# Performance work log

Measured on AMD Instinct MI355X. Metric: run time of the kernel, lower is better.

The kernel has to match this reference:

```python
import jax, jax.numpy as jnp
import numpy as np

B = 131072
MOTION_DIM = 512


def setup_inputs() -> dict:
    key = jax.random.key(0)
    k1, k2 = jax.random.split(key)
    inp = jax.random.normal(k1, (B, MOTION_DIM), dtype=jnp.float32)
    weight = jax.random.normal(k2, (512, MOTION_DIM), dtype=jnp.float32)
    return {"input": inp, "weight": weight}


def reference(input, weight):
    # weight: (512, motion_dim); reduced QR -> Q: (512, motion_dim)
    Q, R = jnp.linalg.qr(weight + 1e-8)
    # Original: sum_i diag(input)[b] @ Q.T over dim=1 == input @ Q.T
    # out[b, n] = sum_m input[b, m] * Q[n, m]
    out = jnp.einsum("bm,nm->bn", input, Q)  # (B, 512)
    return out
```

## Files before the change

### kernel.cpp

```cpp
#include <hip/hip_runtime.h>
#include <hip/hip_bf16.h>

#define NN 512
#define NB 32
#define NPANELS 16
#define BDIM 256
#define PF_BDIM 512
#define LB_BDIM 512


__device__ inline unsigned short f2bf(float x) {
    unsigned int u = __float_as_uint(x);
    return (unsigned short)((u + 0x7FFFu + ((u >> 16) & 1u)) >> 16);
}

__global__ __launch_bounds__(BDIM)
void prep_kernel(const float* __restrict__ W, float* __restrict__ A, float* __restrict__ Q)
{
    int idx = blockIdx.x * BDIM + threadIdx.x;
    if (idx < NN * NN) {
        A[idx] = W[idx] + 1e-8f;
        int r = idx >> 9, c = idx & (NN - 1);
        Q[idx] = (r == c) ? 1.0f : 0.0f;
    }
}

__global__ __launch_bounds__(PF_BDIM)
void panel_fact(float* __restrict__ A, float* __restrict__ Vbuf,
                float* __restrict__ tau, float* __restrict__ Tbuf, int p)
{
    const int k0 = p * NB;
    const int L  = NN - k0;
    const int LP = L + 1;
    __shared__ float sP[NB * (NN + 1)];
    __shared__ float red[PF_BDIM];
    __shared__ float red2[8];
    __shared__ float wbuf[NB];
    __shared__ float sdot[NB];
    __shared__ float sc[2];
    __shared__ float Tt[NB][NB];

    const int t = threadIdx.x;
    const int r = t >> 5;
    const int j = t & 31;

    for (int idx = t; idx < L * NB; idx += PF_BDIM) {
        int i = idx >> 5, jj = idx & 31;
        sP[jj * LP + i] = A[(k0 + i) * NN + (k0 + jj)];
    }
    __syncthreads();

    for (int c = 0; c < NB; ++c) {
        {
            float part = 0.f;
            int i = c + 1 + t;
            if (i < L) {
                float x = sP[c * LP + i];
                part = x * x;
            }
            #pragma unroll
            for (int off = 32; off > 0; off >>= 1)
                part += __shfl_down(part, off, 64);
            if ((t & 63) == 0) red2[t >> 6] = part;
        }
        __syncthreads();
        if (t == 0) {
            float xn2 = 0.f;
            #pragma unroll
            for (int g = 0; g < 8; ++g) xn2 += red2[g];
            float alpha = sP[c * LP + c];
            float tc, inv;
            if (xn2 <= 0.f) { tc = 0.f; inv = 0.f; }
            else {
                float nrm  = sqrtf(alpha * alpha + xn2);
                float beta = (alpha >= 0.f) ? -nrm : nrm;
                tc  = (beta - alpha) / beta;
                inv = 1.f / (alpha - beta);
            }
            sc[0] = tc; sc[1] = inv;
        }
        __syncthreads();
        const float tc = sc[0], inv = sc[1];
        {
            int i = t;
            if (i < L) {
                float x = sP[c * LP + i];
                sP[c * LP + i] = (i > c) ? x * inv : (i == c ? 1.0f : 0.0f);
            }
        }
        __syncthreads();
        {
            float acc = 0.f;
            if (j != c) {
                #pragma unroll 8
                for (int i = r; i < L; i += 16)
                    acc += sP[c * LP + i] * sP[j * LP + i];
            }
            red[t] = acc;
        }
        __syncthreads();
        if (t < NB) {
            float s = 0.f;
            #pragma unroll
            for (int g = 0; g < 16; ++g) s += red[g * NB + t];
            if (t > c)      wbuf[t] = tc * s;
            else if (t < c) sdot[t] = s;
        }
        __syncthreads();
        if (j > c) {
            float wv = wbuf[j];
            #pragma unroll 8
            for (int i = r; i < L; i += 16)
                sP[j * LP + i] -= sP[c * LP + i] * wv;
        }
        if (r == 15) {
            if (j < c) {
                float s = 0.f;
                for (int l = j; l < c; ++l) s += Tt[j][l] * sdot[l];
                Tt[j][c] = -tc * s;
            } else if (j == c) {
                Tt[c][c] = tc;
            }
        }
        __syncthreads();
    }

    for (int idx = t; idx < L * NB; idx += PF_BDIM) {
        int i = idx >> 5, jj = idx & 31;
        Vbuf[p * (NN * NB) + idx] = sP[jj * LP + i];
    }
    for (int q = t; q < NB * NB; q += PF_BDIM) {
        int a = q >> 5, b = q & 31;
        Tbuf[p * (NB * NB) + q] = (a <= b) ? Tt[a][b] : 0.0f;
    }
}

__global__ __launch_bounds__(LB_BDIM)
void larfb_kernel(float* __restrict__ C, const float* __restrict__ Vbuf,
                  const float* __restrict__ Tbuf, int p, int colStart, int transT)
{
    const int k0 = p * NB;
    const int L  = NN - k0;
    const float* Vp = Vbuf + p * (NN * NB);
    const float* Tp = Tbuf + p * (NB * NB);

    __shared__ float sT[NB * NB];
    __shared__ __align__(16) float Vs[NN * NB];
    __shared__ float red[8][64][NB + 1];
    __shared__ float w2s[64][NB + 1];

    const int t   = threadIdx.x;
    const int w   = t >> 6;
    const int jj  = t & 63;
    const int col = colStart + blockIdx.x * 64 + jj;
    const bool valid = col < NN;

    for (int q = t; q < NB * NB; q += LB_BDIM) sT[q] = Tp[q];
    {
        const int nv4 = (L * NB) >> 2;
        const float4* Vp4 = (const float4*)Vp;
        float4* Vs4 = (float4*)Vs;
        for (int q = t; q < nv4; q += LB_BDIM) Vs4[q] = Vp4[q];
    }
    __syncthreads();

    float y[NB];
    #pragma unroll
    for (int m = 0; m < NB; ++m) y[m] = 0.f;
    if (valid) {
        #pragma unroll 4
        for (int i = w; i < L; i += 8) {
            float cij = C[(long)(k0 + i) * NN + col];
            const float4* vr = (const float4*)(Vs + i * NB);
            #pragma unroll
            for (int q4 = 0; q4 < 8; ++q4) {
                float4 v = vr[q4];
                y[4*q4+0] += v.x * cij;
                y[4*q4+1] += v.y * cij;
                y[4*q4+2] += v.z * cij;
                y[4*q4+3] += v.w * cij;
            }
        }
    }
    #pragma unroll
    for (int m = 0; m < NB; ++m) red[w][jj][m] = y[m];
    __syncthreads();
    {
        int jl = t & 63, m0 = (t >> 6) * 4;
        #pragma unroll
        for (int mm = 0; mm < 4; ++mm) {
            int m = m0 + mm;
            float s = red[0][jl][m];
            #pragma unroll
            for (int g = 1; g < 8; ++g) s += red[g][jl][m];
            red[0][jl][m] = s;
        }
    }
    __syncthreads();
    {
        int jl = t & 63, m0 = (t >> 6) * 4;
        #pragma unroll
        for (int mm = 0; mm < 4; ++mm) {
            int m = m0 + mm;
            float s = 0.f;
            #pragma unroll
            for (int l = 0; l < NB; ++l) {
                float tv = transT ? sT[l * NB + m] : sT[m * NB + l];
                s += tv * red[0][jl][l];
            }
            w2s[jl][m] = s;
        }
    }
    __syncthreads();
    if (valid) {
        float w2[NB];
        #pragma unroll
        for (int m = 0; m < NB; ++m) w2[m] = w2s[jj][m];
        #pragma unroll 4
        for (int i = w; i < L; i += 8) {
            const float4* vr = (const float4*)(Vs + i * NB);
            float upd = 0.f;
            #pragma unroll
            for (int q4 = 0; q4 < 8; ++q4) {
                float4 v = vr[q4];
                upd += v.x * w2[4*q4+0] + v.y * w2[4*q4+1]
                     + v.z * w2[4*q4+2] + v.w * w2[4*q4+3];
            }
            C[(long)(k0 + i) * NN + col] -= upd;
        }
    }
}

__global__ __launch_bounds__(BDIM)
void cast_q(const float* __restrict__ Q, unsigned short* __restrict__ Qbf)
{
    int idx = blockIdx.x * BDIM + threadIdx.x;
    if (idx < NN * NN) Qbf[idx] = f2bf(Q[idx]);
}

typedef __bf16 bf16x8 __attribute__((ext_vector_type(8)));
typedef float  f32x4  __attribute__((ext_vector_type(4)));

#define BM 128
#define BN 128
#define BK 32

__global__ __launch_bounds__(BDIM)
void gemm_kernel(const float* __restrict__ Ain, const unsigned short* __restrict__ Bt,
                 float* __restrict__ Cout)
{
    __shared__ unsigned short As[BM * BK];
    __shared__ unsigned short Bs[BN * BK];

    const int t   = threadIdx.x;
    const int bid = (blockIdx.x >> 3) + (blockIdx.x & 7) * (4096 / 8);
    const int nt  = bid & 3;
    const int mt  = bid >> 2;
    const int m0  = mt * BM;
    const int n0  = nt * BN;

    const int lane = t & 63;
    const int wave = t >> 6;
    const int wm = wave >> 1, wn = wave & 1;

    f32x4 acc[4][4];
    #pragma unroll
    for (int a = 0; a < 4; ++a)
        #pragma unroll
        for (int b = 0; b < 4; ++b) acc[a][b] = (f32x4){0.f, 0.f, 0.f, 0.f};

    const int mrow_f = lane & 15;
    const int koff   = (lane >> 4) * 8;

    for (int kk = 0; kk < NN; kk += BK) {
        #pragma unroll
        for (int q = 0; q < 4; ++q) {
            int pidx = t + q * BDIM;
            int mrow = pidx >> 3;
            int kq   = pidx & 7;
            const float4 a4 = *(const float4*)(Ain + (long)(m0 + mrow) * NN + kk + kq * 4);
            ushort4 b4;
            b4.x = f2bf(a4.x); b4.y = f2bf(a4.y); b4.z = f2bf(a4.z); b4.w = f2bf(a4.w);
            *(ushort4*)(&As[mrow * BK + kq * 4]) = b4;
        }
        #pragma unroll
        for (int q = 0; q < 2; ++q) {
            int pidx = t + q * BDIM;
            int nrow = pidx >> 2;
            int k8   = pidx & 3;
            float4 raw = *(const float4*)(Bt + (long)(n0 + nrow) * NN + kk + k8 * 8);
            *(float4*)(&Bs[nrow * BK + k8 * 8]) = raw;
        }
        __syncthreads();

        bf16x8 af[4], bfr[4];
        #pragma unroll
        for (int a = 0; a < 4; ++a)
            af[a] = *(const bf16x8*)(&As[(wm * 64 + a * 16 + mrow_f) * BK + koff]);
        #pragma unroll
        for (int b = 0; b < 4; ++b)
            bfr[b] = *(const bf16x8*)(&Bs[(wn * 64 + b * 16 + mrow_f) * BK + koff]);
        #pragma unroll
        for (int a = 0; a < 4; ++a)
            #pragma unroll
            for (int b = 0; b < 4; ++b)
                acc[a][b] = __builtin_amdgcn_mfma_f32_16x16x32_bf16(af[a], bfr[b], acc[a][b], 0, 0, 0);
        __syncthreads();
    }

    #pragma unroll
    for (int a = 0; a < 4; ++a) {
        int rbase = m0 + wm * 64 + a * 16 + (lane >> 4) * 4;
        #pragma unroll
        for (int b = 0; b < 4; ++b) {
            int cidx = n0 + wn * 64 + b * 16 + (lane & 15);
            #pragma unroll
            for (int r = 0; r < 4; ++r)
                Cout[(long)(rbase + r) * NN + cidx] = acc[a][b][r];
        }
    }
}

extern "C" void kernel_launch(void* const* d_in, const int* in_sizes, int n_in,
                              void* d_out, int out_size, void* d_ws, size_t ws_size,
                              hipStream_t stream)
{
    const float* inp = (const float*)d_in[0];
    const float* wgt = (const float*)d_in[1];
    float* ws  = (float*)d_ws;
    float* A   = ws;
    float* V   = ws + 262144;
    float* tau = ws + 524288;
    float* T   = ws + 524800;
    float* Q   = ws + 541184;
    unsigned short* Qbf = (unsigned short*)(ws + 803328);
    float* out = (float*)d_out;

    prep_kernel<<<(NN * NN + BDIM - 1) / BDIM, BDIM, 0, stream>>>(wgt, A, Q);

    for (int p = 0; p < NPANELS; ++p) {
        panel_fact<<<1, PF_BDIM, 0, stream>>>(A, V, tau, T, p);
        int colStart = p * NB + NB;
        int nc = NN - colStart;
        if (nc > 0)
            larfb_kernel<<<(nc + 63) / 64, LB_BDIM, 0, stream>>>(A, V, T, p, colStart, 1);
    }
    for (int p = NPANELS - 1; p >= 0; --p) {
        int colStart = p * NB;
        int nc = NN - colStart;
        larfb_kernel<<<(nc + 63) / 64, LB_BDIM, 0, stream>>>(Q, V, T, p, colStart, 0);
    }
    cast_q<<<(NN * NN + BDIM - 1) / BDIM, BDIM, 0, stream>>>(Q, Qbf);

    gemm_kernel<<<(131072 / BM) * (NN / BN), BDIM, 0, stream>>>(inp, Qbf, out);
}
```

Before: 2.604 ms.

## Restructure panel factorization, widen larfb columns, fuse bf16 cast, pad GEMM LDS

The panel factorization drops one barrier per column. It folds the column scaling into the dot-product phase and computes the next column's norm during the trailing update. larfb now uses 256 threads with two columns each, loaded as float2. The last Q-application pass writes the bf16 copy directly, so the separate cast kernel is removed. The GEMM pads its LDS rows to a stride of 40 to reduce bank conflicts. Together these change several stages and risk subtle numerical differences in the Householder reformulation.

```diff
diff --git a/kernel.cpp b/kernel.cpp
--- a/kernel.cpp
+++ b/kernel.cpp
@@ -6,7 +6,7 @@
 #define NPANELS 16
 #define BDIM 256
 #define PF_BDIM 512
-#define LB_BDIM 512
+#define LB_BDIM 256
 
 
 __device__ inline unsigned short f2bf(float x) {
@@ -27,14 +27,14 @@
 
 __global__ __launch_bounds__(PF_BDIM)
 void panel_fact(float* __restrict__ A, float* __restrict__ Vbuf,
-                float* __restrict__ tau, float* __restrict__ Tbuf, int p)
+                float* __restrict__ Tbuf, int p)
 {
     const int k0 = p * NB;
     const int L  = NN - k0;
     const int LP = L + 1;
     __shared__ float sP[NB * (NN + 1)];
     __shared__ float red[PF_BDIM];
-    __shared__ float red2[8];
+    __shared__ float red2[16];
     __shared__ float wbuf[NB];
     __shared__ float sdot[NB];
     __shared__ float sc[2];
@@ -50,24 +50,24 @@
     }
     __syncthreads();
 
+    {
+        float part = 0.f;
+        for (int i = 1 + t; i < L; i += PF_BDIM) {
+            float x = sP[i];
+            part += x * x;
+        }
+        #pragma unroll
+        for (int off = 32; off > 0; off >>= 1)
+            part += __shfl_down(part, off, 64);
+        if ((t & 63) == 0) red2[t >> 6] = part;
+    }
+    __syncthreads();
+
     for (int c = 0; c < NB; ++c) {
-        {
-            float part = 0.f;
-            int i = c + 1 + t;
-            if (i < L) {
-                float x = sP[c * LP + i];
-                part = x * x;
-            }
-            #pragma unroll
-            for (int off = 32; off > 0; off >>= 1)
-                part += __shfl_down(part, off, 64);
-            if ((t & 63) == 0) red2[t >> 6] = part;
-        }
-        __syncthreads();
         if (t == 0) {
+            int np = (c == 0) ? 8 : 16;
             float xn2 = 0.f;
-            #pragma unroll
-            for (int g = 0; g < 8; ++g) xn2 += red2[g];
+            for (int g = 0; g < np; ++g) xn2 += red2[g];
             float alpha = sP[c * LP + c];
             float tc, inv;
             if (xn2 <= 0.f) { tc = 0.f; inv = 0.f; }
@@ -81,37 +81,51 @@
         }
         __syncthreads();
         const float tc = sc[0], inv = sc[1];
-        {
-            int i = t;
-            if (i < L) {
-                float x = sP[c * LP + i];
-                sP[c * LP + i] = (i > c) ? x * inv : (i == c ? 1.0f : 0.0f);
-            }
-        }
-        __syncthreads();
+
         {
             float acc = 0.f;
             if (j != c) {
-                #pragma unroll 8
-                for (int i = r; i < L; i += 16)
+                #pragma unroll 4
+                for (int i = c + 1 + r; i < L; i += 16)
                     acc += sP[c * LP + i] * sP[j * LP + i];
             }
             red[t] = acc;
         }
         __syncthreads();
+
         if (t < NB) {
-            float s = 0.f;
-            #pragma unroll
-            for (int g = 0; g < 16; ++g) s += red[g * NB + t];
-            if (t > c)      wbuf[t] = tc * s;
-            else if (t < c) sdot[t] = s;
-        }
-        __syncthreads();
+            if (t != c) {
+                float s = 0.f;
+                #pragma unroll
+                for (int g = 0; g < 16; ++g) s += red[g * NB + t];
+                float val = sP[t * LP + c] + inv * s;
+                if (t > c) wbuf[t] = tc * val;
+                else       sdot[t] = val;
+            }
+        } else {
+            for (int i = t - NB; i < L; i += PF_BDIM - NB) {
+                float x = sP[c * LP + i];
+                sP[c * LP + i] = (i > c) ? x * inv : (i == c ? 1.0f : 0.0f);
+            }
+        }
+        __syncthreads();
+
         if (j > c) {
             float wv = wbuf[j];
-            #pragma unroll 8
-            for (int i = r; i < L; i += 16)
-                sP[j * LP + i] -= sP[c * LP + i] * wv;
+            if (j == c + 1) {
+                float nacc = 0.f;
+                #pragma unroll 4
+                for (int i = c + 1 + r; i < L; i += 16) {
+                    float nv = sP[j * LP + i] - sP[c * LP + i] * wv;
+                    sP[j * LP + i] = nv;
+                    if (i > c + 1) nacc += nv * nv;
+                }
+                red2[r] = nacc;
+            } else {
+                #pragma unroll 4
+                for (int i = c + 1 + r; i < L; i += 16)
+                    sP[j * LP + i] -= sP[c * LP + i] * wv;
+            }
         }
         if (r == 15) {
             if (j < c) {
@@ -137,7 +151,8 @@
 
 __global__ __launch_bounds__(LB_BDIM)
 void larfb_kernel(float* __restrict__ C, const float* __restrict__ Vbuf,
-                  const float* __restrict__ Tbuf, int p, int colStart, int transT)
+                  const float* __restrict__ Tbuf, int p, int colStart, int transT,
+                  int emitBf, unsigned short* __restrict__ Qbf)
 {
     const int k0 = p * NB;
     const int L  = NN - k0;
@@ -149,11 +164,11 @@
     __shared__ float red[8][64][NB + 1];
     __shared__ float w2s[64][NB + 1];
 
-    const int t   = threadIdx.x;
-    const int w   = t >> 6;
-    const int jj  = t & 63;
-    const int col = colStart + blockIdx.x * 64 + jj;
-    const bool valid = col < NN;
+    const int t    = threadIdx.x;
+    const int w    = t >> 5;
+    const int cp   = t & 31;
+    const int col0 = colStart + blockIdx.x * 64 + 2 * cp;
+    const bool valid = col0 < NN;
 
     for (int q = t; q < NB * NB; q += LB_BDIM) sT[q] = Tp[q];
     {
@@ -164,31 +179,34 @@
     }
     __syncthreads();
 
-    float y[NB];
+    float y0[NB], y1[NB];
     #pragma unroll
-    for (int m = 0; m < NB; ++m) y[m] = 0.f;
+    for (int m = 0; m < NB; ++m) { y0[m] = 0.f; y1[m] = 0.f; }
     if (valid) {
-        #pragma unroll 4
+        #pragma unroll 2
         for (int i = w; i < L; i += 8) {
-            float cij = C[(long)(k0 + i) * NN + col];
+            float2 c2 = *(const float2*)(C + (long)(k0 + i) * NN + col0);
             const float4* vr = (const float4*)(Vs + i * NB);
             #pragma unroll
             for (int q4 = 0; q4 < 8; ++q4) {
                 float4 v = vr[q4];
-                y[4*q4+0] += v.x * cij;
-                y[4*q4+1] += v.y * cij;
-                y[4*q4+2] += v.z * cij;
-                y[4*q4+3] += v.w * cij;
+                y0[4*q4+0] += v.x * c2.x;  y1[4*q4+0] += v.x * c2.y;
+                y0[4*q4+1] += v.y * c2.x;  y1[4*q4+1] += v.y * c2.y;
+                y0[4*q4+2] += v.z * c2.x;  y1[4*q4+2] += v.z * c2.y;
+                y0[4*q4+3] += v.w * c2.x;  y1[4*q4+3] += v.w * c2.y;
             }
         }
     }
     #pragma unroll
-    for (int m = 0; m < NB; ++m) red[w][jj][m] = y[m];
+    for (int m = 0; m < NB; ++m) {
+        red[w][2*cp][m]   = y0[m];
+        red[w][2*cp+1][m] = y1[m];
+    }
     __syncthreads();
     {
-        int jl = t & 63, m0 = (t >> 6) * 4;
-        #pragma unroll
-        for (int mm = 0; mm < 4; ++mm) {
+        int jl = t & 63, m0 = (t >> 6) * 8;
+        #pragma unroll
+        for (int mm = 0; mm < 8; ++mm) {
             int m = m0 + mm;
             float s = red[0][jl][m];
             #pragma unroll
@@ -198,9 +216,9 @@
     }
     __syncthreads();
     {
-        int jl = t & 63, m0 = (t >> 6) * 4;
-        #pragma unroll
-        for (int mm = 0; mm < 4; ++mm) {
+        int jl = t & 63, m0 = (t >> 6) * 8;
+        #pragma unroll
+        for (int mm = 0; mm < 8; ++mm) {
             int m = m0 + mm;
             float s = 0.f;
             #pragma unroll
@@ -213,29 +231,31 @@
     }
     __syncthreads();
     if (valid) {
-        float w2[NB];
-        #pragma unroll
-        for (int m = 0; m < NB; ++m) w2[m] = w2s[jj][m];
-        #pragma unroll 4
+        float w20[NB], w21[NB];
+        #pragma unroll
+        for (int m = 0; m < NB; ++m) { w20[m] = w2s[2*cp][m]; w21[m] = w2s[2*cp+1][m]; }
+        #pragma unroll 2
         for (int i = w; i < L; i += 8) {
             const float4* vr = (const float4*)(Vs + i * NB);
-            float upd = 0.f;
+            float u0 = 0.f, u1 = 0.f;
             #pragma unroll
             for (int q4 = 0; q4 < 8; ++q4) {
                 float4 v = vr[q4];
-                upd += v.x * w2[4*q4+0] + v.y * w2[4*q4+1]
-                     + v.z * w2[4*q4+2] + v.w * w2[4*q4+3];
-            }
-            C[(long)(k0 + i) * NN + col] -= upd;
-        }
-    }
-}
-
-__global__ __launch_bounds__(BDIM)
-void cast_q(const float* __restrict__ Q, unsigned short* __restrict__ Qbf)
-{
-    int idx = blockIdx.x * BDIM + threadIdx.x;
-    if (idx < NN * NN) Qbf[idx] = f2bf(Q[idx]);
+                u0 += v.x * w20[4*q4+0] + v.y * w20[4*q4+1]
+                    + v.z * w20[4*q4+2] + v.w * w20[4*q4+3];
+                u1 += v.x * w21[4*q4+0] + v.y * w21[4*q4+1]
+                    + v.z * w21[4*q4+2] + v.w * w21[4*q4+3];
+            }
+            float2* cptr = (float2*)(C + (long)(k0 + i) * NN + col0);
+            float2 old = *cptr;
+            old.x -= u0; old.y -= u1;
+            *cptr = old;
+            if (emitBf) {
+                ushort2 b; b.x = f2bf(old.x); b.y = f2bf(old.y);
+                *(ushort2*)(Qbf + (long)(k0 + i) * NN + col0) = b;
+            }
+        }
+    }
 }
 
 typedef __bf16 bf16x8 __attribute__((ext_vector_type(8)));
@@ -244,13 +264,14 @@
 #define BM 128
 #define BN 128
 #define BK 32
+#define AST 40
 
 __global__ __launch_bounds__(BDIM)
 void gemm_kernel(const float* __restrict__ Ain, const unsigned short* __restrict__ Bt,
                  float* __restrict__ Cout)
 {
-    __shared__ unsigned short As[BM * BK];
-    __shared__ unsigned short Bs[BN * BK];
+    __shared__ __align__(16) unsigned short As[BM * AST];
+    __shared__ __align__(16) unsigned short Bs[BN * AST];
 
     const int t   = threadIdx.x;
     const int bid = (blockIdx.x >> 3) + (blockIdx.x & 7) * (4096 / 8);
@@ -281,7 +302,7 @@
             const float4 a4 = *(const float4*)(Ain + (long)(m0 + mrow) * NN + kk + kq * 4);
             ushort4 b4;
             b4.x = f2bf(a4.x); b4.y = f2bf(a4.y); b4.z = f2bf(a4.z); b4.w = f2bf(a4.w);
-            *(ushort4*)(&As[mrow * BK + kq * 4]) = b4;
+            *(ushort4*)(&As[mrow * AST + kq * 4]) = b4;
         }
         #pragma unroll
         for (int q = 0; q < 2; ++q) {
@@ -289,17 +310,17 @@
             int nrow = pidx >> 2;
             int k8   = pidx & 3;
             float4 raw = *(const float4*)(Bt + (long)(n0 + nrow) * NN + kk + k8 * 8);
-            *(float4*)(&Bs[nrow * BK + k8 * 8]) = raw;
+            *(float4*)(&Bs[nrow * AST + k8 * 8]) = raw;
         }
         __syncthreads();
 
         bf16x8 af[4], bfr[4];
         #pragma unroll
         for (int a = 0; a < 4; ++a)
-            af[a] = *(const bf16x8*)(&As[(wm * 64 + a * 16 + mrow_f) * BK + koff]);
+            af[a] = *(const bf16x8*)(&As[(wm * 64 + a * 16 + mrow_f) * AST + koff]);
         #pragma unroll
         for (int b = 0; b < 4; ++b)
-            bfr[b] = *(const bf16x8*)(&Bs[(wn * 64 + b * 16 + mrow_f) * BK + koff]);
+            bfr[b] = *(const bf16x8*)(&Bs[(wn * 64 + b * 16 + mrow_f) * AST + koff]);
         #pragma unroll
         for (int a = 0; a < 4; ++a)
             #pragma unroll
@@ -330,7 +351,6 @@
     float* ws  = (float*)d_ws;
     float* A   = ws;
     float* V   = ws + 262144;
-    float* tau = ws + 524288;
     float* T   = ws + 524800;
     float* Q   = ws + 541184;
     unsigned short* Qbf = (unsigned short*)(ws + 803328);
@@ -339,18 +359,18 @@
     prep_kernel<<<(NN * NN + BDIM - 1) / BDIM, BDIM, 0, stream>>>(wgt, A, Q);
 
     for (int p = 0; p < NPANELS; ++p) {
-        panel_fact<<<1, PF_BDIM, 0, stream>>>(A, V, tau, T, p);
+        panel_fact<<<1, PF_BDIM, 0, stream>>>(A, V, T, p);
         int colStart = p * NB + NB;
         int nc = NN - colStart;
         if (nc > 0)
-            larfb_kernel<<<(nc + 63) / 64, LB_BDIM, 0, stream>>>(A, V, T, p, colStart, 1);
+            larfb_kernel<<<(nc + 63) / 64, LB_BDIM, 0, stream>>>(A, V, T, p, colStart, 1, 0, nullptr);
     }
     for (int p = NPANELS - 1; p >= 0; --p) {
         int colStart = p * NB;
         int nc = NN - colStart;
-        larfb_kernel<<<(nc + 63) / 64, LB_BDIM, 0, stream>>>(Q, V, T, p, colStart, 0);
-    }
-    cast_q<<<(NN * NN + BDIM - 1) / BDIM, BDIM, 0, stream>>>(Q, Qbf);
+        larfb_kernel<<<(nc + 63) / 64, LB_BDIM, 0, stream>>>(Q, V, T, p, colStart, 0,
+                                                             (p == 0) ? 1 : 0, Qbf);
+    }
 
     gemm_kernel<<<(131072 / BM) * (NN / BN), BDIM, 0, stream>>>(inp, Qbf, out);
 }
```

Result: slower. 3.083 ms (+18.4%).
